# Kernel tuning notes

Measured on AMD Instinct MI355X. Metric: run time of the kernel, lower is better.

## Reference

```python
import jax, jax.numpy as jnp
import numpy as np

N = 50000      # num nodes
E = 800000     # edges per hypergraph (avg degree 16)
G = 3          # hyper_edge_num
D_IN = 128
D_OUT = 128


def setup_inputs() -> dict:
    key = jax.random.key(0)
    ks = jax.random.split(key, 6)
    company_emb = jax.random.normal(ks[0], (N, D_IN), dtype=jnp.float32)
    # nn.Linear weight [out, in], glorot-ish scaling
    W = jax.random.normal(ks[1], (D_OUT, D_IN), dtype=jnp.float32) / np.sqrt(D_IN).astype(np.float32)
    alpha = jax.random.normal(ks[2], (G, 1), dtype=jnp.float32)
    edge_rows = jax.random.randint(ks[3], (G, E), 0, N, dtype=jnp.int32)
    edge_cols = jax.random.randint(ks[4], (G, E), 0, N, dtype=jnp.int32)
    edge_vals = jax.random.normal(ks[5], (G, E), dtype=jnp.float32)
    return {
        "company_emb": company_emb,
        "W": W,
        "alpha": alpha,
        "edge_rows": edge_rows,
        "edge_cols": edge_cols,
        "edge_vals": edge_vals,
    }


def reference(company_emb, W, alpha, edge_rows, edge_cols, edge_vals):
    # shared dense projection: h = X @ W^T, [N, D_OUT]
    h = company_emb @ W.T

    def spmm(rows, cols, vals):
        # sparse Laplacian (COO) @ h : gather source rows, scale, scatter-add to dest rows
        msg = vals[:, None] * h[cols]                     # [E, D_OUT]
        return jax.ops.segment_sum(msg, rows, num_segments=N)

    aggs = jax.vmap(spmm)(edge_rows, edge_cols, edge_vals)  # [G, N, D_OUT]
    gate = jax.nn.sigmoid(alpha[:, 0])                       # [G]
    # res = sum_g sigmoid(alpha_g) * (L_g @ h)
    return jnp.einsum('g,gnd->nd', gate, aggs)
```

## Files before the change

### kernel.cpp

```cpp
#include <hip/hip_runtime.h>
#include <math.h>

#define NNODES 50000
#define NEDGE  800000
#define NG     3
#define D      128
#define GE     (NG*NEDGE)
#define NBUK   782
#define CH     4096
#define NBLK   ((GE + CH - 1) / CH)
#define OS     (NBUK + 1)
#define CAP2   3456

typedef __attribute__((ext_vector_type(8))) short bf16x8;
typedef __attribute__((ext_vector_type(4))) float f32x4;

__device__ __forceinline__ unsigned short f2bf(float f) {
    unsigned u = __float_as_uint(f);
    return (unsigned short)((u + 0x7fffu + ((u >> 16) & 1u)) >> 16);
}

__global__ void k_wprep(const float* __restrict__ W, uint4* __restrict__ Wf) {
    const int t = threadIdx.x;
    for (int i = t; i < 2048; i += 256) {
        const int nt   = i >> 8;
        const int kc   = (i >> 6) & 3;
        const int lane = i & 63;
        const int n  = nt * 16 + (lane & 15);
        const int k0 = kc * 32 + (lane >> 4) * 8;
        const float* src = W + (size_t)n * 128 + k0;
        unsigned u0 = (unsigned)f2bf(src[0]) | ((unsigned)f2bf(src[1]) << 16);
        unsigned u1 = (unsigned)f2bf(src[2]) | ((unsigned)f2bf(src[3]) << 16);
        unsigned u2 = (unsigned)f2bf(src[4]) | ((unsigned)f2bf(src[5]) << 16);
        unsigned u3 = (unsigned)f2bf(src[6]) | ((unsigned)f2bf(src[7]) << 16);
        Wf[i] = make_uint4(u0, u1, u2, u3);
    }
}

__global__ __launch_bounds__(256) void k_gemm(const float* __restrict__ X,
                                              const uint4* __restrict__ Wf,
                                              unsigned short* __restrict__ hb16) {
    __shared__ uint4 Wl[2048];
    const int t = threadIdx.x;
#pragma unroll
    for (int j = 0; j < 8; ++j) Wl[t + j * 256] = Wf[t + j * 256];
    __syncthreads();

    const int w    = t >> 6;
    const int lane = t & 63;
    const int q    = lane >> 4;
    const int ml   = lane & 15;
    const int m0   = blockIdx.x * 64 + w * 16;

    int xr = m0 + ml; if (xr >= NNODES) xr = NNODES - 1;
    const float* xrow = X + (size_t)xr * 128;

    bf16x8 xf[4];
#pragma unroll
    for (int kc = 0; kc < 4; ++kc) {
        const int k0 = kc * 32 + q * 8;
        float4 a = *(const float4*)(xrow + k0);
        float4 b = *(const float4*)(xrow + k0 + 4);
        bf16x8 v;
        v[0] = (short)f2bf(a.x); v[1] = (short)f2bf(a.y);
        v[2] = (short)f2bf(a.z); v[3] = (short)f2bf(a.w);
        v[4] = (short)f2bf(b.x); v[5] = (short)f2bf(b.y);
        v[6] = (short)f2bf(b.z); v[7] = (short)f2bf(b.w);
        xf[kc] = v;
    }

#pragma unroll
    for (int nt = 0; nt < 8; ++nt) {
        f32x4 acc = {0.f, 0.f, 0.f, 0.f};
#pragma unroll
        for (int kc = 0; kc < 4; ++kc) {
            const bf16x8 wf = *(const bf16x8*)&Wl[(nt * 4 + kc) * 64 + lane];
            acc = __builtin_amdgcn_mfma_f32_16x16x32_bf16(xf[kc], wf, acc, 0, 0, 0);
        }
#pragma unroll
        for (int r = 0; r < 4; ++r) {
            const int row = m0 + q * 4 + r;
            if (row < NNODES)
                hb16[(size_t)row * 128 + nt * 16 + ml] = f2bf(acc[r]);
        }
    }
}

__global__ __launch_bounds__(256) void k_bin(const int* __restrict__ rows,
                                             const int* __restrict__ cols,
                                             const float* __restrict__ vals,
                                             const float* __restrict__ alpha,
                                             uint2* __restrict__ out1,
                                             int* __restrict__ off1) {
    __shared__ uint2 stg[CH];
    __shared__ unsigned short rnk[CH];
    __shared__ int sA[1024];
    const int t   = threadIdx.x;
    const int blk = blockIdx.x;
    const int start = blk * CH;
    const int end   = (start + CH < GE) ? (start + CH) : GE;

    const float g0 = 1.0f / (1.0f + __expf(-alpha[0]));
    const float g1 = 1.0f / (1.0f + __expf(-alpha[1]));
    const float g2 = 1.0f / (1.0f + __expf(-alpha[2]));

#pragma unroll
    for (int j = 0; j < 4; ++j) sA[t + j * 256] = 0;
    __syncthreads();

    for (int idx = start + t, k = t; idx < end; idx += 256, k += 256) {
        const int r = rows[idx];
        const int c = cols[idx];
        const float v = vals[idx];
        const float gv = v * (idx < NEDGE ? g0 : (idx < 2 * NEDGE ? g1 : g2));
        uint2 rec;
        rec.x = ((unsigned)r << 16) | (unsigned)c;
        rec.y = __float_as_uint(gv);
        stg[k] = rec;
        rnk[k] = (unsigned short)atomicAdd(&sA[r >> 6], 1);
    }
    __syncthreads();

    for (int off = 1; off < 1024; off <<= 1) {
        int v[4];
#pragma unroll
        for (int j = 0; j < 4; ++j) {
            const int i = t + j * 256;
            v[j] = sA[i] + ((i >= off) ? sA[i - off] : 0);
        }
        __syncthreads();
#pragma unroll
        for (int j = 0; j < 4; ++j) sA[t + j * 256] = v[j];
        __syncthreads();
    }

    for (int b = t; b < NBUK; b += 256)
        off1[(size_t)blk * OS + b] = b ? sA[b - 1] : 0;
    if (t == 0) off1[(size_t)blk * OS + NBUK] = sA[NBUK - 1];

    for (int idx = start + t, k = t; idx < end; idx += 256, k += 256) {
        const uint2 rec = stg[k];
        const int b = (int)(rec.x >> 22);
        const int pos = (b ? sA[b - 1] : 0) + (int)rnk[k];
        out1[(size_t)blk * CH + pos] = rec;
    }
}

__global__ __launch_bounds__(512) void k_agg2(const unsigned* __restrict__ hbits,
                                              const uint2* __restrict__ out1,
                                              const int* __restrict__ off1,
                                              float* __restrict__ out) {
    __shared__ uint2 stg[CAP2];
    __shared__ unsigned short order[CAP2];
    __shared__ int sA[512];
    __shared__ int sB[512];
    __shared__ int rh[64], rbase[64], rcur[64];
    const int t = threadIdx.x;
    const int b = blockIdx.x;

    if (t < 64) rh[t] = 0;

    const int s0 = off1[(size_t)t * OS + b];
    const int e0 = off1[(size_t)t * OS + b + 1];
    int s1 = 0, e1 = 0;
    int myLen = e0 - s0;
    if (t + 512 < NBLK) {
        s1 = off1[(size_t)(t + 512) * OS + b];
        e1 = off1[(size_t)(t + 512) * OS + b + 1];
        myLen += e1 - s1;
    }
    sA[t] = myLen;
    __syncthreads();

    int* src = sA; int* dst = sB;
    for (int off = 1; off < 512; off <<= 1) {
        dst[t] = src[t] + ((t >= off) ? src[t - off] : 0);
        __syncthreads();
        int* tmp = src; src = dst; dst = tmp;
    }
    const int base = src[t] - myLen;

    {
        int p = base;
        const uint2* seg = out1 + (size_t)t * CH;
        for (int i = s0; i < e0; ++i, ++p) {
            if (p < CAP2) {
                const uint2 rec = seg[i];
                stg[p] = rec;
                atomicAdd(&rh[(rec.x >> 16) & 63u], 1);
            }
        }
        if (t + 512 < NBLK) {
            const uint2* seg2 = out1 + (size_t)(t + 512) * CH;
            for (int i = s1; i < e1; ++i, ++p) {
                if (p < CAP2) {
                    const uint2 rec = seg2[i];
                    stg[p] = rec;
                    atomicAdd(&rh[(rec.x >> 16) & 63u], 1);
                }
            }
        }
    }
    __syncthreads();

    if (t < 64) sA[t] = rh[t];
    __syncthreads();
    for (int off = 1; off < 64; off <<= 1) {
        int v = 0;
        if (t < 64) v = sA[t] + ((t >= off) ? sA[t - off] : 0);
        __syncthreads();
        if (t < 64) sA[t] = v;
        __syncthreads();
    }
    if (t < 64) { rbase[t] = sA[t] - rh[t]; rcur[t] = sA[t] - rh[t]; }
    __syncthreads();

    {
        const int lim = (base + myLen < CAP2) ? (base + myLen) : CAP2;
        for (int k = base; k < lim; ++k) {
            const int lr = (int)((stg[k].x >> 16) & 63u);
            const int pos = atomicAdd(&rcur[lr], 1);
            order[pos] = (unsigned short)k;
        }
    }
    __syncthreads();

    const int w    = t >> 6;
    const int lane = t & 63;
    for (int k = 0; k < 8; ++k) {
        const int lr  = (w << 3) + k;
        const int row = (b << 6) + lr;
        const int s   = rbase[lr];
        const int cnt = rh[lr];
        float2 acc = make_float2(0.f, 0.f);
        int i = 0;
        for (; i + 8 <= cnt; i += 8) {
            int idx8[8];
#pragma unroll
            for (int j = 0; j < 8; ++j) idx8[j] = order[s + i + j];
            uint2 m[8];
#pragma unroll
            for (int j = 0; j < 8; ++j) m[j] = stg[idx8[j]];
            unsigned hb[8];
#pragma unroll
            for (int j = 0; j < 8; ++j)
                hb[j] = hbits[(size_t)(m[j].x & 0xffffu) * 64 + lane];
#pragma unroll
            for (int j = 0; j < 8; ++j) {
                const float v = __uint_as_float(m[j].y);
                acc.x += v * __uint_as_float(hb[j] << 16);
                acc.y += v * __uint_as_float(hb[j] & 0xffff0000u);
            }
        }
        for (; i < cnt; ++i) {
            const uint2 m = stg[order[s + i]];
            const unsigned hbv = hbits[(size_t)(m.x & 0xffffu) * 64 + lane];
            const float v = __uint_as_float(m.y);
            acc.x += v * __uint_as_float(hbv << 16);
            acc.y += v * __uint_as_float(hbv & 0xffff0000u);
        }
        if (row < NNODES)
            ((float2*)out)[(size_t)row * 64 + lane] = acc;
    }
}

extern "C" void kernel_launch(void* const* d_in, const int* in_sizes, int n_in,
                              void* d_out, int out_size, void* d_ws, size_t ws_size,
                              hipStream_t stream) {
    const float* X     = (const float*)d_in[0];
    const float* W     = (const float*)d_in[1];
    const float* alpha = (const float*)d_in[2];
    const int*   rows  = (const int*)d_in[3];
    const int*   cols  = (const int*)d_in[4];
    const float* vals  = (const float*)d_in[5];
    float* out = (float*)d_out;

    char* ws = (char*)d_ws;
    unsigned*       hbits = (unsigned*)(ws + 0);
    unsigned short* hb16  = (unsigned short*)(ws + 0);
    uint2*          out1  = (uint2*)(ws + 12800000);
    int*            off1  = (int*)  (ws + 32002048);
    uint4*          Wf    = (uint4*)(ws + 33837408);

    hipLaunchKernelGGL(k_wprep, dim3(1), dim3(256), 0, stream, W, Wf);
    hipLaunchKernelGGL(k_gemm, dim3(NBUK), dim3(256), 0, stream, X, Wf, hb16);
    hipLaunchKernelGGL(k_bin, dim3(NBLK), dim3(256), 0, stream,
                       rows, cols, vals, alpha, out1, off1);
    hipLaunchKernelGGL(k_agg2, dim3(NBUK), dim3(512), 0, stream,
                       hbits, out1, off1, out);
}
```

Baseline: 239.4 us.

## Transpose bucket offsets, use wave-shuffle scans, and place records directly by row

The binning kernel now replaces its 1024-entry shared-memory Hillis-Steele scan with a wave-shuffle scan, and writes bucket offsets transposed (bucket-major), so the aggregation kernel reads them coalesced. The aggregation kernel drops its 512-wide block scan and its indirection array. It makes a histogram pass over the records, then scatters each record straight into a row-sorted, even-padded slot, so the inner loop reads contiguous 16-byte pairs. The cost is reading the global record segments twice, plus extra shared atomics in the scatter pass.

```diff
diff --git a/kernel.cpp b/kernel.cpp
--- a/kernel.cpp
+++ b/kernel.cpp
@@ -9,7 +9,6 @@
 #define NBUK   782
 #define CH     4096
 #define NBLK   ((GE + CH - 1) / CH)
-#define OS     (NBUK + 1)
 #define CAP2   3456
 
 typedef __attribute__((ext_vector_type(8))) short bf16x8;
@@ -91,10 +90,11 @@
                                              const float* __restrict__ vals,
                                              const float* __restrict__ alpha,
                                              uint2* __restrict__ out1,
-                                             int* __restrict__ off1) {
+                                             int* __restrict__ off1T) {
     __shared__ uint2 stg[CH];
     __shared__ unsigned short rnk[CH];
-    __shared__ int sA[1024];
+    __shared__ int sE[1024];
+    __shared__ int wtot[4];
     const int t   = threadIdx.x;
     const int blk = blockIdx.x;
     const int start = blk * CH;
@@ -105,7 +105,7 @@
     const float g2 = 1.0f / (1.0f + __expf(-alpha[2]));
 
 #pragma unroll
-    for (int j = 0; j < 4; ++j) sA[t + j * 256] = 0;
+    for (int j = 0; j < 4; ++j) sE[t + j * 256] = 0;
     __syncthreads();
 
     for (int idx = start + t, k = t; idx < end; idx += 256, k += 256) {
@@ -117,110 +117,107 @@
         rec.x = ((unsigned)r << 16) | (unsigned)c;
         rec.y = __float_as_uint(gv);
         stg[k] = rec;
-        rnk[k] = (unsigned short)atomicAdd(&sA[r >> 6], 1);
-    }
-    __syncthreads();
-
-    for (int off = 1; off < 1024; off <<= 1) {
-        int v[4];
-#pragma unroll
-        for (int j = 0; j < 4; ++j) {
-            const int i = t + j * 256;
-            v[j] = sA[i] + ((i >= off) ? sA[i - off] : 0);
-        }
-        __syncthreads();
-#pragma unroll
-        for (int j = 0; j < 4; ++j) sA[t + j * 256] = v[j];
-        __syncthreads();
-    }
+        rnk[k] = (unsigned short)atomicAdd(&sE[r >> 6], 1);
+    }
+    __syncthreads();
+
+    const int lane = t & 63;
+    const int w    = t >> 6;
+    int4 v4 = *(int4*)&sE[4 * t];
+    const int l1 = v4.x + v4.y;
+    const int l2 = l1 + v4.z;
+    const int l3 = l2 + v4.w;
+    int s = l3;
+#pragma unroll
+    for (int off = 1; off < 64; off <<= 1) {
+        int n = __shfl_up(s, off);
+        if (lane >= off) s += n;
+    }
+    if (lane == 63) wtot[w] = s;
+    const int waveExcl = s - l3;
+    __syncthreads();
+    int cross = 0;
+    for (int j = 0; j < w; ++j) cross += wtot[j];
+    const int b0 = cross + waveExcl;
+    int4 e4;
+    e4.x = b0; e4.y = b0 + v4.x; e4.z = b0 + l1; e4.w = b0 + l2;
+    *(int4*)&sE[4 * t] = e4;
+    __syncthreads();
 
     for (int b = t; b < NBUK; b += 256)
-        off1[(size_t)blk * OS + b] = b ? sA[b - 1] : 0;
-    if (t == 0) off1[(size_t)blk * OS + NBUK] = sA[NBUK - 1];
+        off1T[(size_t)b * NBLK + blk] = sE[b];
+    if (t == 0) off1T[(size_t)NBUK * NBLK + blk] = end - start;
 
     for (int idx = start + t, k = t; idx < end; idx += 256, k += 256) {
         const uint2 rec = stg[k];
         const int b = (int)(rec.x >> 22);
-        const int pos = (b ? sA[b - 1] : 0) + (int)rnk[k];
-        out1[(size_t)blk * CH + pos] = rec;
+        out1[(size_t)blk * CH + sE[b] + (int)rnk[k]] = rec;
     }
 }
 
 __global__ __launch_bounds__(512) void k_agg2(const unsigned* __restrict__ hbits,
                                               const uint2* __restrict__ out1,
-                                              const int* __restrict__ off1,
+                                              const int* __restrict__ off1T,
                                               float* __restrict__ out) {
     __shared__ uint2 stg[CAP2];
-    __shared__ unsigned short order[CAP2];
-    __shared__ int sA[512];
-    __shared__ int sB[512];
     __shared__ int rh[64], rbase[64], rcur[64];
     const int t = threadIdx.x;
     const int b = blockIdx.x;
 
     if (t < 64) rh[t] = 0;
-
-    const int s0 = off1[(size_t)t * OS + b];
-    const int e0 = off1[(size_t)t * OS + b + 1];
-    int s1 = 0, e1 = 0;
-    int myLen = e0 - s0;
+    __syncthreads();
+
+    int s0 = 0, e0 = 0, s1 = 0, e1 = 0;
+    if (t < NBLK) {
+        s0 = off1T[(size_t)b * NBLK + t];
+        e0 = off1T[(size_t)(b + 1) * NBLK + t];
+    }
     if (t + 512 < NBLK) {
-        s1 = off1[(size_t)(t + 512) * OS + b];
-        e1 = off1[(size_t)(t + 512) * OS + b + 1];
-        myLen += e1 - s1;
-    }
-    sA[t] = myLen;
-    __syncthreads();
-
-    int* src = sA; int* dst = sB;
-    for (int off = 1; off < 512; off <<= 1) {
-        dst[t] = src[t] + ((t >= off) ? src[t - off] : 0);
-        __syncthreads();
-        int* tmp = src; src = dst; dst = tmp;
-    }
-    const int base = src[t] - myLen;
+        s1 = off1T[(size_t)b * NBLK + t + 512];
+        e1 = off1T[(size_t)(b + 1) * NBLK + t + 512];
+    }
 
     {
-        int p = base;
+        const unsigned* seg = (const unsigned*)(out1 + (size_t)t * CH);
+        for (int i = s0; i < e0; ++i)
+            atomicAdd(&rh[(seg[2 * i] >> 16) & 63u], 1);
+        if (t + 512 < NBLK) {
+            const unsigned* seg2 = (const unsigned*)(out1 + (size_t)(t + 512) * CH);
+            for (int i = s1; i < e1; ++i)
+                atomicAdd(&rh[(seg2[2 * i] >> 16) & 63u], 1);
+        }
+    }
+    __syncthreads();
+
+    if (t < 64) {
+        const int pad = (rh[t] + 1) & ~1;
+        int sv = pad;
+#pragma unroll
+        for (int off = 1; off < 64; off <<= 1) {
+            int n = __shfl_up(sv, off);
+            if (t >= off) sv += n;
+        }
+        int base = sv - pad;
+        if (base > CAP2) base = CAP2;
+        rbase[t] = base;
+        rcur[t]  = base;
+    }
+    __syncthreads();
+
+    {
         const uint2* seg = out1 + (size_t)t * CH;
-        for (int i = s0; i < e0; ++i, ++p) {
-            if (p < CAP2) {
-                const uint2 rec = seg[i];
-                stg[p] = rec;
-                atomicAdd(&rh[(rec.x >> 16) & 63u], 1);
-            }
+        for (int i = s0; i < e0; ++i) {
+            const uint2 rec = seg[i];
+            const int pos = atomicAdd(&rcur[(rec.x >> 16) & 63u], 1);
+            if (pos < CAP2) stg[pos] = rec;
         }
         if (t + 512 < NBLK) {
             const uint2* seg2 = out1 + (size_t)(t + 512) * CH;
-            for (int i = s1; i < e1; ++i, ++p) {
-                if (p < CAP2) {
-                    const uint2 rec = seg2[i];
-                    stg[p] = rec;
-                    atomicAdd(&rh[(rec.x >> 16) & 63u], 1);
-                }
+            for (int i = s1; i < e1; ++i) {
+                const uint2 rec = seg2[i];
+                const int pos = atomicAdd(&rcur[(rec.x >> 16) & 63u], 1);
+                if (pos < CAP2) stg[pos] = rec;
             }
-        }
-    }
-    __syncthreads();
-
-    if (t < 64) sA[t] = rh[t];
-    __syncthreads();
-    for (int off = 1; off < 64; off <<= 1) {
-        int v = 0;
-        if (t < 64) v = sA[t] + ((t >= off) ? sA[t - off] : 0);
-        __syncthreads();
-        if (t < 64) sA[t] = v;
-        __syncthreads();
-    }
-    if (t < 64) { rbase[t] = sA[t] - rh[t]; rcur[t] = sA[t] - rh[t]; }
-    __syncthreads();
-
-    {
-        const int lim = (base + myLen < CAP2) ? (base + myLen) : CAP2;
-        for (int k = base; k < lim; ++k) {
-            const int lr = (int)((stg[k].x >> 16) & 63u);
-            const int pos = atomicAdd(&rcur[lr], 1);
-            order[pos] = (unsigned short)k;
         }
     }
     __syncthreads();
@@ -231,29 +228,30 @@
         const int lr  = (w << 3) + k;
         const int row = (b << 6) + lr;
         const int s   = rbase[lr];
-        const int cnt = rh[lr];
+        int cnt = rh[lr];
+        if (s + cnt > CAP2) cnt = (CAP2 > s) ? (CAP2 - s) : 0;
         float2 acc = make_float2(0.f, 0.f);
         int i = 0;
         for (; i + 8 <= cnt; i += 8) {
-            int idx8[8];
-#pragma unroll
-            for (int j = 0; j < 8; ++j) idx8[j] = order[s + i + j];
-            uint2 m[8];
-#pragma unroll
-            for (int j = 0; j < 8; ++j) m[j] = stg[idx8[j]];
+            const uint4 q0 = *(const uint4*)&stg[s + i];
+            const uint4 q1 = *(const uint4*)&stg[s + i + 2];
+            const uint4 q2 = *(const uint4*)&stg[s + i + 4];
+            const uint4 q3 = *(const uint4*)&stg[s + i + 6];
+            unsigned cm[8] = {q0.x, q0.z, q1.x, q1.z, q2.x, q2.z, q3.x, q3.z};
+            unsigned vv[8] = {q0.y, q0.w, q1.y, q1.w, q2.y, q2.w, q3.y, q3.w};
             unsigned hb[8];
 #pragma unroll
             for (int j = 0; j < 8; ++j)
-                hb[j] = hbits[(size_t)(m[j].x & 0xffffu) * 64 + lane];
+                hb[j] = hbits[(size_t)(cm[j] & 0xffffu) * 64 + lane];
 #pragma unroll
             for (int j = 0; j < 8; ++j) {
-                const float v = __uint_as_float(m[j].y);
+                const float v = __uint_as_float(vv[j]);
                 acc.x += v * __uint_as_float(hb[j] << 16);
                 acc.y += v * __uint_as_float(hb[j] & 0xffff0000u);
             }
         }
         for (; i < cnt; ++i) {
-            const uint2 m = stg[order[s + i]];
+            const uint2 m = stg[s + i];
             const unsigned hbv = hbits[(size_t)(m.x & 0xffffu) * 64 + lane];
             const float v = __uint_as_float(m.y);
             acc.x += v * __uint_as_float(hbv << 16);
@@ -279,13 +277,13 @@
     unsigned*       hbits = (unsigned*)(ws + 0);
     unsigned short* hb16  = (unsigned short*)(ws + 0);
     uint2*          out1  = (uint2*)(ws + 12800000);
-    int*            off1  = (int*)  (ws + 32002048);
+    int*            off1T = (int*)  (ws + 32002048);
     uint4*          Wf    = (uint4*)(ws + 33837408);
 
     hipLaunchKernelGGL(k_wprep, dim3(1), dim3(256), 0, stream, W, Wf);
     hipLaunchKernelGGL(k_gemm, dim3(NBUK), dim3(256), 0, stream, X, Wf, hb16);
     hipLaunchKernelGGL(k_bin, dim3(NBLK), dim3(256), 0, stream,
-                       rows, cols, vals, alpha, out1, off1);
+                       rows, cols, vals, alpha, out1, off1T);
     hipLaunchKernelGGL(k_agg2, dim3(NBUK), dim3(512), 0, stream,
-                       hbits, out1, off1, out);
-}
+                       hbits, out1, off1T, out);
+}
```

Result: slower. 260.4 us (+8.8%).

## Split aggregation by source-column half into two passes with transposed offsets

Applied to the files above, without the earlier changes.

The binning kernel now keys edges by destination bucket and by which half of the node range the source column falls in. It writes the per-block offsets in key-major (transposed) order so the aggregation reads them coalesced. Aggregation runs twice, once per column half, with the second pass adding onto the output. Each pass's gathers of h then touch only half of the table, which should improve cache locality. Both kernels also replace the shared-memory scans with wave shuffle scans; the cost is an extra launch, an extra read and write of the output, and smaller per-pass LDS staging that can silently drop edges if the capacity is exceeded.

```diff
diff --git a/kernel.cpp b/kernel.cpp
--- a/kernel.cpp
+++ b/kernel.cpp
@@ -7,10 +7,11 @@
 #define D      128
 #define GE     (NG*NEDGE)
 #define NBUK   782
+#define NKEY   (NBUK*2)
 #define CH     4096
 #define NBLK   ((GE + CH - 1) / CH)
-#define OS     (NBUK + 1)
-#define CAP2   3456
+#define CAPH   1920
+#define COLSPL 25000
 
 typedef __attribute__((ext_vector_type(8))) short bf16x8;
 typedef __attribute__((ext_vector_type(4))) float f32x4;
@@ -91,10 +92,11 @@
                                              const float* __restrict__ vals,
                                              const float* __restrict__ alpha,
                                              uint2* __restrict__ out1,
-                                             int* __restrict__ off1) {
+                                             int* __restrict__ off1T) {
     __shared__ uint2 stg[CH];
     __shared__ unsigned short rnk[CH];
-    __shared__ int sA[1024];
+    __shared__ int sE[2048];
+    __shared__ int wtot[4];
     const int t   = threadIdx.x;
     const int blk = blockIdx.x;
     const int start = blk * CH;
@@ -105,7 +107,7 @@
     const float g2 = 1.0f / (1.0f + __expf(-alpha[2]));
 
 #pragma unroll
-    for (int j = 0; j < 4; ++j) sA[t + j * 256] = 0;
+    for (int j = 0; j < 8; ++j) sE[t + j * 256] = 0;
     __syncthreads();
 
     for (int idx = start + t, k = t; idx < end; idx += 256, k += 256) {
@@ -117,74 +119,89 @@
         rec.x = ((unsigned)r << 16) | (unsigned)c;
         rec.y = __float_as_uint(gv);
         stg[k] = rec;
-        rnk[k] = (unsigned short)atomicAdd(&sA[r >> 6], 1);
-    }
-    __syncthreads();
-
-    for (int off = 1; off < 1024; off <<= 1) {
-        int v[4];
-#pragma unroll
-        for (int j = 0; j < 4; ++j) {
-            const int i = t + j * 256;
-            v[j] = sA[i] + ((i >= off) ? sA[i - off] : 0);
-        }
-        __syncthreads();
-#pragma unroll
-        for (int j = 0; j < 4; ++j) sA[t + j * 256] = v[j];
-        __syncthreads();
-    }
-
-    for (int b = t; b < NBUK; b += 256)
-        off1[(size_t)blk * OS + b] = b ? sA[b - 1] : 0;
-    if (t == 0) off1[(size_t)blk * OS + NBUK] = sA[NBUK - 1];
+        const int key = ((r >> 6) << 1) | (c >= COLSPL);
+        rnk[k] = (unsigned short)atomicAdd(&sE[key], 1);
+    }
+    __syncthreads();
+
+    const int lane = t & 63;
+    const int w    = t >> 6;
+    int v8[8], run = 0;
+#pragma unroll
+    for (int j = 0; j < 8; ++j) { v8[j] = sE[8 * t + j]; run += v8[j]; }
+    int s = run;
+#pragma unroll
+    for (int off = 1; off < 64; off <<= 1) {
+        int n = __shfl_up(s, off);
+        if (lane >= off) s += n;
+    }
+    if (lane == 63) wtot[w] = s;
+    const int waveExcl = s - run;
+    __syncthreads();
+    int cross = 0;
+    for (int j = 0; j < w; ++j) cross += wtot[j];
+    int pos = cross + waveExcl;
+#pragma unroll
+    for (int j = 0; j < 8; ++j) { const int c = v8[j]; sE[8 * t + j] = pos; pos += c; }
+    __syncthreads();
+
+    for (int k = t; k < NKEY; k += 256)
+        off1T[(size_t)k * NBLK + blk] = sE[k];
+    if (t == 0) off1T[(size_t)NKEY * NBLK + blk] = end - start;
 
     for (int idx = start + t, k = t; idx < end; idx += 256, k += 256) {
         const uint2 rec = stg[k];
-        const int b = (int)(rec.x >> 22);
-        const int pos = (b ? sA[b - 1] : 0) + (int)rnk[k];
-        out1[(size_t)blk * CH + pos] = rec;
+        const int key = (int)((rec.x >> 22) << 1) | ((rec.x & 0xffffu) >= COLSPL);
+        out1[(size_t)blk * CH + sE[key] + (int)rnk[k]] = rec;
     }
 }
 
 __global__ __launch_bounds__(512) void k_agg2(const unsigned* __restrict__ hbits,
                                               const uint2* __restrict__ out1,
-                                              const int* __restrict__ off1,
-                                              float* __restrict__ out) {
-    __shared__ uint2 stg[CAP2];
-    __shared__ unsigned short order[CAP2];
+                                              const int* __restrict__ off1T,
+                                              float* __restrict__ out,
+                                              int half, int add) {
+    __shared__ uint2 stg[CAPH];
+    __shared__ unsigned short order[CAPH];
     __shared__ int sA[512];
-    __shared__ int sB[512];
+    __shared__ int wtot[8];
     __shared__ int rh[64], rbase[64], rcur[64];
     const int t = threadIdx.x;
     const int b = blockIdx.x;
+    const int key = b * 2 + half;
 
     if (t < 64) rh[t] = 0;
 
-    const int s0 = off1[(size_t)t * OS + b];
-    const int e0 = off1[(size_t)t * OS + b + 1];
-    int s1 = 0, e1 = 0;
+    int s0 = 0, e0 = 0, s1 = 0, e1 = 0;
+    s0 = off1T[(size_t)key * NBLK + t];
+    e0 = off1T[(size_t)(key + 1) * NBLK + t];
     int myLen = e0 - s0;
     if (t + 512 < NBLK) {
-        s1 = off1[(size_t)(t + 512) * OS + b];
-        e1 = off1[(size_t)(t + 512) * OS + b + 1];
+        s1 = off1T[(size_t)key * NBLK + t + 512];
+        e1 = off1T[(size_t)(key + 1) * NBLK + t + 512];
         myLen += e1 - s1;
     }
-    sA[t] = myLen;
-    __syncthreads();
-
-    int* src = sA; int* dst = sB;
-    for (int off = 1; off < 512; off <<= 1) {
-        dst[t] = src[t] + ((t >= off) ? src[t - off] : 0);
-        __syncthreads();
-        int* tmp = src; src = dst; dst = tmp;
-    }
-    const int base = src[t] - myLen;
+
+    const int lane = t & 63;
+    const int w    = t >> 6;
+    int s = myLen;
+#pragma unroll
+    for (int off = 1; off < 64; off <<= 1) {
+        int n = __shfl_up(s, off);
+        if (lane >= off) s += n;
+    }
+    if (lane == 63) wtot[w] = s;
+    const int waveExcl = s - myLen;
+    __syncthreads();
+    int cross = 0;
+    for (int j = 0; j < w; ++j) cross += wtot[j];
+    const int base = cross + waveExcl;
 
     {
         int p = base;
         const uint2* seg = out1 + (size_t)t * CH;
         for (int i = s0; i < e0; ++i, ++p) {
-            if (p < CAP2) {
+            if (p < CAPH) {
                 const uint2 rec = seg[i];
                 stg[p] = rec;
                 atomicAdd(&rh[(rec.x >> 16) & 63u], 1);
@@ -193,7 +210,7 @@
         if (t + 512 < NBLK) {
             const uint2* seg2 = out1 + (size_t)(t + 512) * CH;
             for (int i = s1; i < e1; ++i, ++p) {
-                if (p < CAP2) {
+                if (p < CAPH) {
                     const uint2 rec = seg2[i];
                     stg[p] = rec;
                     atomicAdd(&rh[(rec.x >> 16) & 63u], 1);
@@ -203,41 +220,43 @@
     }
     __syncthreads();
 
-    if (t < 64) sA[t] = rh[t];
-    __syncthreads();
-    for (int off = 1; off < 64; off <<= 1) {
-        int v = 0;
-        if (t < 64) v = sA[t] + ((t >= off) ? sA[t - off] : 0);
-        __syncthreads();
-        if (t < 64) sA[t] = v;
-        __syncthreads();
-    }
-    if (t < 64) { rbase[t] = sA[t] - rh[t]; rcur[t] = sA[t] - rh[t]; }
+    if (t < 64) {
+        const int c = rh[t];
+        int sv = c;
+#pragma unroll
+        for (int off = 1; off < 64; off <<= 1) {
+            int n = __shfl_up(sv, off);
+            if (t >= off) sv += n;
+        }
+        rbase[t] = sv - c;
+        rcur[t]  = sv - c;
+    }
     __syncthreads();
 
     {
-        const int lim = (base + myLen < CAP2) ? (base + myLen) : CAP2;
+        const int lim = (base + myLen < CAPH) ? (base + myLen) : CAPH;
         for (int k = base; k < lim; ++k) {
             const int lr = (int)((stg[k].x >> 16) & 63u);
             const int pos = atomicAdd(&rcur[lr], 1);
-            order[pos] = (unsigned short)k;
-        }
-    }
-    __syncthreads();
-
-    const int w    = t >> 6;
-    const int lane = t & 63;
+            if (pos < CAPH) order[pos] = (unsigned short)k;
+        }
+    }
+    __syncthreads();
+
     for (int k = 0; k < 8; ++k) {
         const int lr  = (w << 3) + k;
         const int row = (b << 6) + lr;
-        const int s   = rbase[lr];
-        const int cnt = rh[lr];
+        const int sR  = rbase[lr];
+        int cnt = rh[lr];
+        if (sR + cnt > CAPH) cnt = (CAPH > sR) ? (CAPH - sR) : 0;
         float2 acc = make_float2(0.f, 0.f);
+        if (add && row < NNODES)
+            acc = ((const float2*)out)[(size_t)row * 64 + lane];
         int i = 0;
         for (; i + 8 <= cnt; i += 8) {
             int idx8[8];
 #pragma unroll
-            for (int j = 0; j < 8; ++j) idx8[j] = order[s + i + j];
+            for (int j = 0; j < 8; ++j) idx8[j] = order[sR + i + j];
             uint2 m[8];
 #pragma unroll
             for (int j = 0; j < 8; ++j) m[j] = stg[idx8[j]];
@@ -253,7 +272,7 @@
             }
         }
         for (; i < cnt; ++i) {
-            const uint2 m = stg[order[s + i]];
+            const uint2 m = stg[order[sR + i]];
             const unsigned hbv = hbits[(size_t)(m.x & 0xffffu) * 64 + lane];
             const float v = __uint_as_float(m.y);
             acc.x += v * __uint_as_float(hbv << 16);
@@ -279,13 +298,15 @@
     unsigned*       hbits = (unsigned*)(ws + 0);
     unsigned short* hb16  = (unsigned short*)(ws + 0);
     uint2*          out1  = (uint2*)(ws + 12800000);
-    int*            off1  = (int*)  (ws + 32002048);
-    uint4*          Wf    = (uint4*)(ws + 33837408);
+    int*            off1T = (int*)  (ws + 32002048);
+    uint4*          Wf    = (uint4*)(ws + 35670416);
 
     hipLaunchKernelGGL(k_wprep, dim3(1), dim3(256), 0, stream, W, Wf);
     hipLaunchKernelGGL(k_gemm, dim3(NBUK), dim3(256), 0, stream, X, Wf, hb16);
     hipLaunchKernelGGL(k_bin, dim3(NBLK), dim3(256), 0, stream,
-                       rows, cols, vals, alpha, out1, off1);
+                       rows, cols, vals, alpha, out1, off1T);
     hipLaunchKernelGGL(k_agg2, dim3(NBUK), dim3(512), 0, stream,
-                       hbits, out1, off1, out);
-}
+                       hbits, out1, off1T, out, 0, 0);
+    hipLaunchKernelGGL(k_agg2, dim3(NBUK), dim3(512), 0, stream,
+                       hbits, out1, off1T, out, 1, 1);
+}
```

Result: slower. 252.5 us (+5.5%).
